# Kernel optimization log

Hardware: AMD Instinct MI355X
Metric: run time of the kernel (lower is better)

The kernel has to match this reference:

```python
import jax, jax.numpy as jnp
import numpy as np

VIEW_NUM = 360
CHAN_NUM = 512
BATCH = 2
IMG = 512


def setup_inputs() -> dict:
    key = jax.random.key(0)
    x = jax.random.normal(key, (BATCH, 1, IMG, IMG), dtype=jnp.float32)
    return {"x": x}


def _bilinear_sample_zeros(img, ix, iy):
    """Bilinear sample img (B,1,H,W) at pixel coords ix, iy (H,W), zeros padding.
    Matches F.grid_sample(mode='bilinear', padding_mode='zeros', align_corners=False)."""
    H, W = img.shape[-2], img.shape[-1]
    x0 = jnp.floor(ix)
    y0 = jnp.floor(iy)
    x1 = x0 + 1.0
    y1 = y0 + 1.0
    wx1 = ix - x0
    wx0 = 1.0 - wx1
    wy1 = iy - y0
    wy0 = 1.0 - wy1

    def gather(yy, xx):
        valid = (xx >= 0) & (xx <= W - 1) & (yy >= 0) & (yy <= H - 1)
        xi = jnp.clip(xx, 0, W - 1).astype(jnp.int32)
        yi = jnp.clip(yy, 0, H - 1).astype(jnp.int32)
        # fancy-index over spatial dims -> (B,1,H,W)
        return img[:, :, yi, xi] * valid.astype(img.dtype)

    return (gather(y0, x0) * (wy0 * wx0)
            + gather(y0, x1) * (wy0 * wx1)
            + gather(y1, x0) * (wy1 * wx0)
            + gather(y1, x1) * (wy1 * wx1))


def _fp(x):
    B, C, H, W = x.shape
    # affine_grid base coords, align_corners=False: (2i+1)/N - 1
    bx = (2.0 * jnp.arange(W, dtype=x.dtype) + 1.0) / W - 1.0
    by = (2.0 * jnp.arange(H, dtype=x.dtype) + 1.0) / H - 1.0
    X = bx[None, :]  # (1,W)
    Y = by[:, None]  # (H,1)
    i = jnp.arange(VIEW_NUM, dtype=x.dtype)
    angles = -jnp.pi * (i + 1.0) / VIEW_NUM - jnp.pi
    cosv = jnp.cos(angles)
    sinv = jnp.sin(angles)

    def per_view(carry, cs):
        c, s = cs
        # theta = [[c,-s,0],[s,c,0]]; grid = base @ theta^T
        gx = c * X - s * Y  # (H,W) normalized sample x
        gy = s * X + c * Y  # (H,W) normalized sample y
        # unnormalize (align_corners=False)
        ix = ((gx + 1.0) * W - 1.0) * 0.5
        iy = ((gy + 1.0) * H - 1.0) * 0.5
        samp = _bilinear_sample_zeros(x, ix, iy)  # (B,1,H,W)
        return carry, jnp.sum(samp, axis=2)  # sum over height -> (B,1,W)

    _, cols = jax.lax.scan(per_view, 0, (cosv, sinv))  # (V,B,1,W)
    sino = jnp.transpose(cols, (1, 2, 3, 0)) * 0.5  # (B,1,chanNum,viewNum)
    return sino


def reference(x):
    return _fp(x)
```

## Files before the change

### kernel.cpp

```cpp
#include <hip/hip_runtime.h>

typedef __fp16 h2 __attribute__((ext_vector_type(2)));

constexpr int VIEWS = 360;
constexpr int IMGSZ = 512;
constexpr int WCHUNK = 64;
constexpr int KH = 64;
constexpr int NXF4 = 25;
constexpr int PITCH = 100;
constexpr int MAXNY = 94;
constexpr int PW = 712;
constexpr int PH = 704;
constexpr int PAD = 96;

__global__ __launch_bounds__(256) void pad_kernel(const float* __restrict__ x,
                                                  unsigned* __restrict__ padq) {
    constexpr int PW4 = PW / 4;
    constexpr int total = PH * PW4;
    int idx = blockIdx.x * 256 + threadIdx.x;
    if (idx >= total) return;
    int py = idx / PW4;
    int px4 = idx - py * PW4;
    int gx = px4 * 4 - PAD;
    int gy = py - PAD;
    const float* img0 = x;
    const float* img1 = x + (size_t)IMGSZ * IMGSZ;
    float4 a = make_float4(0.f, 0.f, 0.f, 0.f);
    float4 bq = a;
    if ((unsigned)gy < (unsigned)IMGSZ && (unsigned)gx < (unsigned)IMGSZ) {
        size_t off = (size_t)gy * IMGSZ + gx;
        a  = *(const float4*)(img0 + off);
        bq = *(const float4*)(img1 + off);
    }
    uint4 d;
    d.x = __builtin_bit_cast(unsigned, __builtin_amdgcn_cvt_pkrtz(a.x, bq.x));
    d.y = __builtin_bit_cast(unsigned, __builtin_amdgcn_cvt_pkrtz(a.y, bq.y));
    d.z = __builtin_bit_cast(unsigned, __builtin_amdgcn_cvt_pkrtz(a.z, bq.z));
    d.w = __builtin_bit_cast(unsigned, __builtin_amdgcn_cvt_pkrtz(a.w, bq.w));
    *(uint4*)&padq[(size_t)idx * 4] = d;
}

__device__ __forceinline__ h2 dpp_reduce_add_h2(h2 x) {
    h2 acc = x;
#define DPP_STEP(ctrl)                                                      \
    {                                                                       \
        int t = __builtin_amdgcn_update_dpp(                                \
            0, (int)__builtin_bit_cast(unsigned, acc), (ctrl), 0xf, 0xf,    \
            true);                                                          \
        acc = acc + __builtin_bit_cast(h2, (unsigned)t);                    \
    }
    DPP_STEP(0x111)
    DPP_STEP(0x112)
    DPP_STEP(0x114)
    DPP_STEP(0x118)
    DPP_STEP(0x142)
    DPP_STEP(0x143)
#undef DPP_STEP
    return acc;
}

__device__ __forceinline__ void gatomic_fadd(float* p, float v) {
    asm volatile("global_atomic_add_f32 %0, %1, off" : : "v"(p), "v"(v)
                 : "memory");
}

__global__ __launch_bounds__(256, 4) void fp_kernel(const unsigned* __restrict__ padq,
                                                    float* __restrict__ out) {
    __shared__ __align__(16) unsigned tileU[PITCH * MAXNY];

    int blk = blockIdx.x;
    int wc = blk & 7;
    int v = blk >> 3;
    int vj = v + 180;

    int tid = threadIdx.x;
    int lane = tid & 63;
    int g = tid >> 6;
    int w = wc * WCHUNK + lane;

    double ang = -3.14159265358979323846 * (double)(v + 1) / (double)VIEWS
                 - 3.14159265358979323846;
    float c = (float)cos(ang);
    float s = (float)sin(ang);

    float xw = (float)w + 0.5f - 256.0f;
    float cxw = fmaf(c, xw, 255.5f);
    float sxw = fmaf(s, xw, 255.5f);

    float lo = -1e30f, hi = 1e30f;
    {
        float coef = -s, base = cxw;
        if (fabsf(coef) > 1e-6f) {
            float a = (-1.0f - base) / coef;
            float bq = (512.0f - base) / coef;
            lo = fmaxf(lo, fminf(a, bq));
            hi = fminf(hi, fmaxf(a, bq));
        } else if (!(base > -1.0f && base < 512.0f)) {
            lo = 1e30f; hi = -1e30f;
        }
    }
    {
        float coef = c, base = sxw;
        if (fabsf(coef) > 1e-6f) {
            float a = (-1.0f - base) / coef;
            float bq = (512.0f - base) / coef;
            lo = fmaxf(lo, fminf(a, bq));
            hi = fminf(hi, fmaxf(a, bq));
        } else if (!(base > -1.0f && base < 512.0f)) {
            lo = 1e30f; hi = -1e30f;
        }
    }
    float h0f = fminf(fmaxf(floorf(lo + 255.5f) - 1.0f, 0.0f), 512.0f);
    float h1f = fminf(fmaxf(ceilf(hi + 255.5f) + 1.0f, -1.0f), 511.0f);
    int h0 = (int)h0f;
    int h1 = (int)h1f;

    int bh0 = h0, bh1 = h1;
    #pragma unroll
    for (int m = 1; m < 64; m <<= 1) {
        bh0 = min(bh0, __shfl_xor(bh0, m, 64));
        bh1 = max(bh1, __shfl_xor(bh1, m, 64));
    }

    float xa = (float)(wc * WCHUNK) + 0.5f - 256.0f;
    float xb = xa + 63.0f;

    float acc0 = 0.0f, acc1 = 0.0f;
    float step4x = -4.0f * s;
    float step4y = 4.0f * c;

    for (int hc = bh0; hc <= bh1; hc += KH) {
        int hend = min(hc + KH - 1, bh1);

        float ha = (float)hc - 255.5f;
        float hb = (float)hend - 255.5f;
        float ix00 = c * xa - s * ha, ix01 = c * xa - s * hb;
        float ix10 = c * xb - s * ha, ix11 = c * xb - s * hb;
        float iy00 = s * xa + c * ha, iy01 = s * xa + c * hb;
        float iy10 = s * xb + c * ha, iy11 = s * xb + c * hb;
        float ixmn = fminf(fminf(ix00, ix01), fminf(ix10, ix11)) + 255.5f;
        float iymn = fminf(fminf(iy00, iy01), fminf(iy10, iy11)) + 255.5f;
        float iymx = fmaxf(fmaxf(iy00, iy01), fmaxf(iy10, iy11)) + 255.5f;
        int x_lo = (int)floorf(ixmn) - 1;
        int x_lo4 = x_lo & ~3;
        int y_lo = (int)floorf(iymn) - 1;
        int NY = min((int)floorf(iymx) + 3 - y_lo, MAXNY);
        int total4 = NY * NXF4;
        int nit = (total4 + 255) >> 8;

        __syncthreads();

        {
            const unsigned* pb = padq + (y_lo + PAD) * PW + (x_lo4 + PAD);
            for (int k = 0; k < nit; ++k) {
                int ic = min((k << 8) + tid, total4 - 1);
                int ry = ic / NXF4;
                uint4 val = *(const uint4*)(pb + 4 * ic + (PW - 4 * NXF4) * ry);
                *(uint4*)&tileU[ic << 2] = val;
            }
        }
        __syncthreads();

        float hh0 = (float)(hc + g) - 255.5f;
        float ixr = fmaf(-s, hh0, cxw) - (float)x_lo4;
        float iyr = fmaf(c, hh0, sxw) - (float)y_lo;
        h2 accp0 = (h2)0.0f;
        h2 accp1 = (h2)0.0f;
        int parity = 0;
        #pragma unroll 8
        for (int h = hc + g; h <= hend; h += 4) {
            float tx = truncf(ixr);
            float ty = truncf(iyr);
            float wx1 = ixr - tx;
            float wy1 = iyr - ty;
            h2 wxs = __builtin_amdgcn_cvt_pkrtz(wx1, wx1);
            h2 wys = __builtin_amdgcn_cvt_pkrtz(wy1, wy1);
            unsigned a = (unsigned)fmaf(ty, 400.0f, tx * 4.0f);
            const unsigned* p = (const unsigned*)((const char*)tileU + a);
            h2 t00 = __builtin_bit_cast(h2, p[0]);
            h2 t01 = __builtin_bit_cast(h2, p[1]);
            h2 t10 = __builtin_bit_cast(h2, p[PITCH]);
            h2 t11 = __builtin_bit_cast(h2, p[PITCH + 1]);
            h2 r0 = t00 + (t01 - t00) * wxs;
            h2 r1 = t10 + (t11 - t10) * wxs;
            h2 contrib = r0 + (r1 - r0) * wys;
            if (parity) accp1 += contrib; else accp0 += contrib;
            parity ^= 1;
            h2 red = dpp_reduce_add_h2(contrib);
            if (lane == 63 && __builtin_bit_cast(unsigned, red) != 0u) {
                float* p0 = out + ((size_t)(511 - h) * VIEWS + vj);
                gatomic_fadd(p0, (float)red.x * 0.5f);
                gatomic_fadd(p0 + (size_t)IMGSZ * VIEWS, (float)red.y * 0.5f);
            }
            ixr += step4x;
            iyr += step4y;
        }
        acc0 += (float)accp0.x + (float)accp1.x;
        acc1 += (float)accp0.y + (float)accp1.y;
    }

    __syncthreads();
    tileU[(g << 6) + lane] = __float_as_uint(acc0);
    tileU[256 + (g << 6) + lane] = __float_as_uint(acc1);
    __syncthreads();
    if (g == 0) {
        float r0 = __uint_as_float(tileU[lane]) + __uint_as_float(tileU[64 + lane]) +
                   __uint_as_float(tileU[128 + lane]) + __uint_as_float(tileU[192 + lane]);
        float r1 = __uint_as_float(tileU[256 + lane]) + __uint_as_float(tileU[320 + lane]) +
                   __uint_as_float(tileU[384 + lane]) + __uint_as_float(tileU[448 + lane]);
        size_t o = (size_t)w * VIEWS + v;
        out[o] = r0 * 0.5f;
        out[(size_t)IMGSZ * VIEWS + o] = r1 * 0.5f;
    }
}

extern "C" void kernel_launch(void* const* d_in, const int* in_sizes, int n_in,
                              void* d_out, int out_size, void* d_ws, size_t ws_size,
                              hipStream_t stream) {
    const float* x = (const float*)d_in[0];
    float* out = (float*)d_out;
    unsigned* padq = (unsigned*)d_ws;

    constexpr int padTotal = PH * (PW / 4);
    pad_kernel<<<(padTotal + 255) / 256, 256, 0, stream>>>(x, padq);

    int nblocks = (VIEWS / 2) * (IMGSZ / WCHUNK);
    fp_kernel<<<nblocks, 256, 0, stream>>>(padq, out);
}
```

Before: 180.9 us.

## Batch per-row column reductions via DPP groups and LDS instead of per-iteration wave reduce

The inner sampling loop is fully unrolled to 16 fixed iterations, each guarded by a bounds check. Per-iteration contributions are kept in registers. The old 6-step full-wave DPP reduction and single-lane atomic in every iteration are replaced by a 4-step row reduction per iteration, a cross-row combine through a small LDS buffer, and atomics spread across 16 lanes. LDS addresses are clamped so that out-of-range unrolled iterations stay safe. The aim is to cut serialized DPP work and atomic issue from the hot loop, at the cost of more registers (16 h2 accumulators) and extra LDS traffic. The memory clobber is also dropped from the atomic asm.

```diff
diff --git a/kernel.cpp b/kernel.cpp
--- a/kernel.cpp
+++ b/kernel.cpp
@@ -9,9 +9,11 @@
 constexpr int NXF4 = 25;
 constexpr int PITCH = 100;
 constexpr int MAXNY = 94;
+constexpr int LDSDW = PITCH * MAXNY;
 constexpr int PW = 712;
 constexpr int PH = 704;
 constexpr int PAD = 96;
+constexpr unsigned MAXA = (unsigned)(LDSDW - PITCH - 2) * 4u;
 
 __global__ __launch_bounds__(256) void pad_kernel(const float* __restrict__ x,
                                                   unsigned* __restrict__ padq) {
@@ -40,33 +42,29 @@
     *(uint4*)&padq[(size_t)idx * 4] = d;
 }
 
-__device__ __forceinline__ h2 dpp_reduce_add_h2(h2 x) {
-    h2 acc = x;
-#define DPP_STEP(ctrl)                                                      \
-    {                                                                       \
-        int t = __builtin_amdgcn_update_dpp(                                \
-            0, (int)__builtin_bit_cast(unsigned, acc), (ctrl), 0xf, 0xf,    \
-            true);                                                          \
-        acc = acc + __builtin_bit_cast(h2, (unsigned)t);                    \
-    }
-    DPP_STEP(0x111)
-    DPP_STEP(0x112)
-    DPP_STEP(0x114)
-    DPP_STEP(0x118)
-    DPP_STEP(0x142)
-    DPP_STEP(0x143)
-#undef DPP_STEP
-    return acc;
-}
-
 __device__ __forceinline__ void gatomic_fadd(float* p, float v) {
-    asm volatile("global_atomic_add_f32 %0, %1, off" : : "v"(p), "v"(v)
-                 : "memory");
+    asm volatile("global_atomic_add_f32 %0, %1, off" : : "v"(p), "v"(v));
+}
+
+template <int CTRL>
+__device__ __forceinline__ h2 dpp_add_step(h2 acc) {
+    int t = __builtin_amdgcn_update_dpp(
+        0, (int)__builtin_bit_cast(unsigned, acc), CTRL, 0xf, 0xf, true);
+    return acc + __builtin_bit_cast(h2, (unsigned)t);
+}
+
+__device__ __forceinline__ h2 dpp_group_reduce(h2 x) {
+    x = dpp_add_step<0x111>(x);
+    x = dpp_add_step<0x112>(x);
+    x = dpp_add_step<0x114>(x);
+    x = dpp_add_step<0x118>(x);
+    return x;
 }
 
 __global__ __launch_bounds__(256, 4) void fp_kernel(const unsigned* __restrict__ padq,
                                                     float* __restrict__ out) {
-    __shared__ __align__(16) unsigned tileU[PITCH * MAXNY];
+    __shared__ __align__(16) unsigned tileU[LDSDW];
+    __shared__ __align__(16) unsigned colLds[4 * 16 * 4];
 
     int blk = blockIdx.x;
     int wc = blk & 7;
@@ -166,9 +164,11 @@
         float iyr = fmaf(c, hh0, sxw) - (float)y_lo;
         h2 accp0 = (h2)0.0f;
         h2 accp1 = (h2)0.0f;
-        int parity = 0;
-        #pragma unroll 8
-        for (int h = hc + g; h <= hend; h += 4) {
+        h2 colA[16];
+        #pragma unroll
+        for (int t = 0; t < 16; ++t) colA[t] = (h2)0.0f;
+        #pragma unroll
+        for (int t = 0; t < 16; ++t) {
             float tx = truncf(ixr);
             float ty = truncf(iyr);
             float wx1 = ixr - tx;
@@ -176,6 +176,7 @@
             h2 wxs = __builtin_amdgcn_cvt_pkrtz(wx1, wx1);
             h2 wys = __builtin_amdgcn_cvt_pkrtz(wy1, wy1);
             unsigned a = (unsigned)fmaf(ty, 400.0f, tx * 4.0f);
+            a = min(a, MAXA);
             const unsigned* p = (const unsigned*)((const char*)tileU + a);
             h2 t00 = __builtin_bit_cast(h2, p[0]);
             h2 t01 = __builtin_bit_cast(h2, p[1]);
@@ -184,19 +185,40 @@
             h2 r0 = t00 + (t01 - t00) * wxs;
             h2 r1 = t10 + (t11 - t10) * wxs;
             h2 contrib = r0 + (r1 - r0) * wys;
-            if (parity) accp1 += contrib; else accp0 += contrib;
-            parity ^= 1;
-            h2 red = dpp_reduce_add_h2(contrib);
-            if (lane == 63 && __builtin_bit_cast(unsigned, red) != 0u) {
-                float* p0 = out + ((size_t)(511 - h) * VIEWS + vj);
-                gatomic_fadd(p0, (float)red.x * 0.5f);
-                gatomic_fadd(p0 + (size_t)IMGSZ * VIEWS, (float)red.y * 0.5f);
+            if (hc + g + 4 * t <= hend) {
+                if (t & 1) accp1 += contrib; else accp0 += contrib;
+                colA[t] = contrib;
             }
             ixr += step4x;
             iyr += step4y;
         }
         acc0 += (float)accp0.x + (float)accp1.x;
         acc1 += (float)accp0.y + (float)accp1.y;
+
+        #pragma unroll
+        for (int t = 0; t < 16; ++t) colA[t] = dpp_group_reduce(colA[t]);
+
+        {
+            unsigned* cl = colLds + (g << 6);
+            int grp = lane >> 4;
+            if ((lane & 15) == 15) {
+                #pragma unroll
+                for (int t = 0; t < 16; ++t)
+                    cl[(t << 2) + grp] = __builtin_bit_cast(unsigned, colA[t]);
+            }
+            int h = hc + g + 4 * lane;
+            if (lane < 16 && h <= hend) {
+                uint4 q = *(const uint4*)&cl[lane << 2];
+                h2 sA = __builtin_bit_cast(h2, q.x) + __builtin_bit_cast(h2, q.y);
+                h2 sB = __builtin_bit_cast(h2, q.z) + __builtin_bit_cast(h2, q.w);
+                h2 red = sA + sB;
+                if (__builtin_bit_cast(unsigned, red) != 0u) {
+                    float* p0 = out + ((size_t)(511 - h) * VIEWS + vj);
+                    gatomic_fadd(p0, (float)red.x * 0.5f);
+                    gatomic_fadd(p0 + (size_t)IMGSZ * VIEWS, (float)red.y * 0.5f);
+                }
+            }
+        }
     }
 
     __syncthreads();
```

Result: no change. 182.4 us (+0.8%).
